# Performance work log

Measured on AMD Instinct MI355X. Metric: run time of the kernel, lower is better.

## Reference

```python
import jax, jax.numpy as jnp
import numpy as np

B, S, D, H = 4, 2048, 512, 8
HD = D // H  # head_size = 64


def setup_inputs() -> dict:
    key = jax.random.key(0)
    ks = jax.random.split(key, 11)
    sd = 1.0 / np.sqrt(D)
    return {
        "q": jax.random.normal(ks[0], (B, S, D), jnp.float32),
        "k": jax.random.normal(ks[1], (B, S, D), jnp.float32),
        "v": jax.random.normal(ks[2], (B, S, D), jnp.float32),
        "Wq": jax.random.normal(ks[3], (D, D), jnp.float32) * sd,
        "bq": jnp.zeros((D,), jnp.float32),
        "Wk": jax.random.normal(ks[4], (D, D), jnp.float32) * sd,
        "bk": jnp.zeros((D,), jnp.float32),
        "Wv": jax.random.normal(ks[5], (D, D), jnp.float32) * sd,
        "bv": jnp.zeros((D,), jnp.float32),
        "Wo": jax.random.normal(ks[6], (D, D), jnp.float32) * sd,
        "bo": jnp.zeros((D,), jnp.float32),
    }


def _split_heads(x):
    # [B,S,D] -> [B,H,S,HD]
    return x.reshape(B, S, H, HD).transpose(0, 2, 1, 3)


def reference(q, k, v, Wq, bq, Wk, bk, Wv, bv, Wo, bo):
    qp = _split_heads(q @ Wq.T + bq)
    kp = _split_heads(k @ Wk.T + bk)
    vp = _split_heads(v @ Wv.T + bv)
    scale = 1.0 / jnp.sqrt(jnp.float32(HD))
    scores = jnp.einsum("bhqd,bhkd->bhqk", qp, kp) * scale  # [B,H,S,S]
    weights = jax.nn.softmax(scores, axis=-1)
    ctx = jnp.einsum("bhqk,bhkd->bhqd", weights, vp)
    ctx = ctx.transpose(0, 2, 1, 3).reshape(B, S, D)
    return ctx @ Wo.T + bo
```

## Files before the change

### kernel.cpp

```cpp
#include <hip/hip_runtime.h>
#include <hip/hip_bf16.h>
#include <stdint.h>

#define BB   4
#define SS   2048
#define DDIM 512
#define HH   8
#define HDIM 64
#define MTOT (BB*SS)
#define QSCALE (0.125f * 1.44269504088896340736f)

typedef __bf16 bf16;
typedef __bf16 bf16x8 __attribute__((ext_vector_type(8)));
typedef float  f32x4  __attribute__((ext_vector_type(4)));

__device__ __forceinline__ void gload_lds16(const void* g, void* l) {
    __builtin_amdgcn_global_load_lds(
        (__attribute__((address_space(1))) unsigned int*)(uintptr_t)g,
        (__attribute__((address_space(3))) unsigned int*)l,
        16, 0, 0);
}

__global__ void cvt_kernel(const float* __restrict__ s0, const float* __restrict__ s1,
                           const float* __restrict__ s2, const float* __restrict__ s3,
                           bf16* __restrict__ d0, bf16* __restrict__ d1,
                           bf16* __restrict__ d2, bf16* __restrict__ d3, int n4) {
    const float* s; bf16* d;
    switch (blockIdx.y) {
        case 0:  s = s0; d = d0; break;
        case 1:  s = s1; d = d1; break;
        case 2:  s = s2; d = d2; break;
        default: s = s3; d = d3; break;
    }
    int stride = gridDim.x * blockDim.x;
    for (int i = blockIdx.x * blockDim.x + threadIdx.x; i < n4; i += stride) {
        float4 f = ((const float4*)s)[i];
        union { bf16 h[4]; uint2 u; } o;
        o.h[0] = (bf16)f.x; o.h[1] = (bf16)f.y; o.h[2] = (bf16)f.z; o.h[3] = (bf16)f.w;
        ((uint2*)d)[i] = o.u;
    }
}

#define GEMM_BODY(A_, W_, K_)                                                    \
    __shared__ bf16 As[128 * 32];                                                \
    __shared__ bf16 Bs[128 * 32];                                                \
    const int tid = threadIdx.x;                                                 \
    const int w = tid >> 6, lane = tid & 63;                                     \
    const int c15 = lane & 15, quad = lane >> 4;                                 \
    const int mblk = blockIdx.x * 128, nblk = blockIdx.y * 128;                  \
    const int wm = (w & 1) * 64, wn = (w >> 1) * 64;                             \
    f32x4 acc[4][4] = {};                                                        \
    const bf16* Ablk = (A_) + (size_t)mblk * (K_);                               \
    const bf16* Bblk = (W_) + (size_t)nblk * (K_);                               \
    const int srow = w * 32 + (lane >> 2);                                       \
    const int scol = (lane & 3) * 8;                                             \
    for (int kt = 0; kt < (K_); kt += 32) {                                      \
        __syncthreads();                                                         \
        gload_lds16(Ablk + (size_t)srow * (K_) + kt + scol, &As[(w*32) * 32]);   \
        gload_lds16(Ablk + (size_t)(srow+16) * (K_) + kt + scol, &As[(w*32+16)*32]); \
        gload_lds16(Bblk + (size_t)srow * (K_) + kt + scol, &Bs[(w*32) * 32]);   \
        gload_lds16(Bblk + (size_t)(srow+16) * (K_) + kt + scol, &Bs[(w*32+16)*32]); \
        __syncthreads();                                                         \
        bf16x8 af[4], bfr[4];                                                    \
        _Pragma("unroll")                                                        \
        for (int i = 0; i < 4; ++i)                                              \
            af[i] = *(const bf16x8*)&As[(wm + i*16 + c15) * 32 + quad * 8];      \
        _Pragma("unroll")                                                        \
        for (int j = 0; j < 4; ++j)                                              \
            bfr[j] = *(const bf16x8*)&Bs[(wn + j*16 + c15) * 32 + quad * 8];     \
        _Pragma("unroll")                                                        \
        for (int i = 0; i < 4; ++i)                                              \
            _Pragma("unroll")                                                    \
            for (int j = 0; j < 4; ++j)                                          \
                acc[i][j] = __builtin_amdgcn_mfma_f32_16x16x32_bf16(             \
                    af[i], bfr[j], acc[i][j], 0, 0, 0);                          \
    }

__global__ __launch_bounds__(256)
void proj_gemm(const bf16* __restrict__ Aq, const bf16* __restrict__ Ak,
               const bf16* __restrict__ Wq, const bf16* __restrict__ Wk,
               const float* __restrict__ bq, const float* __restrict__ bk,
               bf16* __restrict__ Qp, bf16* __restrict__ Kp) {
    const int mode = blockIdx.z;
    const bf16* A  = mode ? Ak : Aq;
    const bf16* Wm = mode ? Wk : Wq;
    const float* bias = mode ? bk : bq;
    GEMM_BODY(A, Wm, DDIM)
    #pragma unroll
    for (int j = 0; j < 4; ++j) {
        const int col = nblk + wn + j * 16 + c15;
        const int h = col >> 6, hd = col & 63;
        const float bval = bias[col];
        #pragma unroll
        for (int i = 0; i < 4; ++i) {
            #pragma unroll
            for (int r = 0; r < 4; ++r) {
                const int row = mblk + wm + i * 16 + quad * 4 + r;
                const int b = row >> 11, s = row & (SS - 1);
                float v = acc[i][j][r] + bval;
                if (mode == 0) {
                    v *= QSCALE;
                    Qp[(((size_t)(b * HH + h)) * SS + s) * HDIM + hd] = (bf16)v;
                } else {
                    Kp[(((size_t)(b * HH + h)) * SS + s) * HDIM + hd] = (bf16)v;
                }
            }
        }
    }
}

__global__ __launch_bounds__(256)
void projv_gemm(const bf16* __restrict__ Wv, const bf16* __restrict__ Av,
                const float* __restrict__ bv, bf16* __restrict__ Vt2) {
    GEMM_BODY(Wv, Av, DDIM)
    #pragma unroll
    for (int i = 0; i < 4; ++i) {
        #pragma unroll
        for (int r = 0; r < 4; ++r) {
            const int row = mblk + wm + i * 16 + quad * 4 + r;
            const float bval = bv[row];
            #pragma unroll
            for (int j = 0; j < 4; ++j) {
                const int col = nblk + wn + j * 16 + c15;
                Vt2[(size_t)row * MTOT + col] = (bf16)(acc[i][j][r] + bval);
            }
        }
    }
}

__global__ __launch_bounds__(256)
void out_gemm(const bf16* __restrict__ A, const bf16* __restrict__ Wo,
              const float* __restrict__ bo, float* __restrict__ Out) {
    GEMM_BODY(A, Wo, DDIM)
    #pragma unroll
    for (int j = 0; j < 4; ++j) {
        const int col = nblk + wn + j * 16 + c15;
        const float bval = bo[col];
        #pragma unroll
        for (int i = 0; i < 4; ++i) {
            #pragma unroll
            for (int r = 0; r < 4; ++r) {
                const int row = mblk + wm + i * 16 + quad * 4 + r;
                Out[(size_t)row * DDIM + col] = acc[i][j][r] + bval;
            }
        }
    }
}

__global__ __launch_bounds__(256, 2)
void attn_kernel(const bf16* __restrict__ Qp, const bf16* __restrict__ Kp,
                 const bf16* __restrict__ Vt2, bf16* __restrict__ Ctx) {
    __shared__ bf16 Klds[128 * 64];
    __shared__ bf16 Vlds[64 * 128];
    __shared__ bf16 Plds[4][32 * 128];

    const int tid = threadIdx.x;
    const int w = tid >> 6, lane = tid & 63;
    const int c15 = lane & 15, quad = lane >> 4;
    const int bh = blockIdx.y;
    const int b = bh >> 3, h = bh & 7;
    const int qbase = blockIdx.x * 128;

    const bf16* Qh = Qp + (size_t)bh * SS * HDIM;
    const bf16* Kh = Kp + (size_t)bh * SS * HDIM;
    const bf16* Vh = Vt2 + (size_t)h * HDIM * MTOT + (size_t)b * SS;

    bf16x8 qf[2][2];
    #pragma unroll
    for (int g = 0; g < 2; ++g) {
        const int qrow = qbase + w * 32 + g * 16 + c15;
        qf[g][0] = *(const bf16x8*)&Qh[(size_t)qrow * HDIM + quad * 8];
        qf[g][1] = *(const bf16x8*)&Qh[(size_t)qrow * HDIM + 32 + quad * 8];
    }

    int koff[4], voff[4];
    #pragma unroll
    for (int ci = 0; ci < 4; ++ci) {
        const int s = (w * 4 + ci) * 64 + lane;
        const int kr = s >> 3, kc = (s & 7) ^ (kr & 7);
        koff[ci] = kr * HDIM + kc * 8;
        const int vr = s >> 4, vc = (s & 15) ^ (vr & 15);
        voff[ci] = vr * MTOT + vc * 8;
    }

    f32x4 oacc[2][4] = {};
    f32x4 lacc[2] = {};
    const bf16 one = (bf16)1.0f;
    const bf16x8 ones = {one, one, one, one, one, one, one, one};
    bf16* Pw = &Plds[w][0];
    const int ksw = c15 & 7;

    for (int kt = 0; kt < SS; kt += 128) {
        __syncthreads();
        const bf16* Ks = Kh + (size_t)kt * HDIM;
        const bf16* Vs = Vh + kt;
        #pragma unroll
        for (int ci = 0; ci < 4; ++ci)
            gload_lds16(Ks + koff[ci], &Klds[(w * 4 + ci) * 512]);
        #pragma unroll
        for (int ci = 0; ci < 4; ++ci)
            gload_lds16(Vs + voff[ci], &Vlds[(w * 4 + ci) * 512]);
        __syncthreads();

        f32x4 sc[2][8];
        #pragma unroll
        for (int nt = 0; nt < 8; ++nt) {
            const int krow = nt * 16 + c15;
            bf16x8 kb0 = *(const bf16x8*)&Klds[(krow * 8 + (quad ^ ksw)) * 8];
            bf16x8 kb1 = *(const bf16x8*)&Klds[(krow * 8 + ((quad + 4) ^ ksw)) * 8];
            #pragma unroll
            for (int g = 0; g < 2; ++g) {
                f32x4 z = {};
                z = __builtin_amdgcn_mfma_f32_16x16x32_bf16(qf[g][0], kb0, z, 0, 0, 0);
                z = __builtin_amdgcn_mfma_f32_16x16x32_bf16(qf[g][1], kb1, z, 0, 0, 0);
                sc[g][nt] = z;
            }
        }

        #pragma unroll
        for (int g = 0; g < 2; ++g)
            #pragma unroll
            for (int nt = 0; nt < 8; ++nt)
                #pragma unroll
                for (int r = 0; r < 4; ++r) {
                    const float p = __builtin_amdgcn_exp2f(sc[g][nt][r]);
                    const int rm = quad * 4 + r;
                    Pw[(g * 16 + rm) * 128 + (((nt * 2 + (c15 >> 3)) ^ rm) * 8) + (c15 & 7)] = (bf16)p;
                }

        bf16x8 pa[2][4];
        #pragma unroll
        for (int g = 0; g < 2; ++g)
            #pragma unroll
            for (int c = 0; c < 4; ++c)
                pa[g][c] = *(const bf16x8*)&Pw[(g * 16 + c15) * 128 + ((c * 4 + quad) ^ c15) * 8];

        #pragma unroll
        for (int g = 0; g < 2; ++g)
            #pragma unroll
            for (int c = 0; c < 4; ++c)
                lacc[g] = __builtin_amdgcn_mfma_f32_16x16x32_bf16(pa[g][c], ones, lacc[g], 0, 0, 0);

        #pragma unroll
        for (int c = 0; c < 4; ++c) {
            #pragma unroll
            for (int j = 0; j < 4; ++j) {
                const int vrow = j * 16 + c15;
                bf16x8 vb = *(const bf16x8*)&Vlds[vrow * 128 + ((c * 4 + quad) ^ c15) * 8];
                oacc[0][j] = __builtin_amdgcn_mfma_f32_16x16x32_bf16(pa[0][c], vb, oacc[0][j], 0, 0, 0);
                oacc[1][j] = __builtin_amdgcn_mfma_f32_16x16x32_bf16(pa[1][c], vb, oacc[1][j], 0, 0, 0);
            }
        }
    }

    bf16* Cb = Ctx + ((size_t)b * SS) * DDIM + (size_t)h * HDIM;
    #pragma unroll
    for (int g = 0; g < 2; ++g)
        #pragma unroll
        for (int r = 0; r < 4; ++r) {
            const int row = qbase + w * 32 + g * 16 + quad * 4 + r;
            const float inv = 1.0f / lacc[g][r];
            #pragma unroll
            for (int j = 0; j < 4; ++j) {
                const int hd = j * 16 + c15;
                Cb[(size_t)row * DDIM + hd] = (bf16)(oacc[g][j][r] * inv);
            }
        }
}

extern "C" void kernel_launch(void* const* d_in, const int* in_sizes, int n_in,
                              void* d_out, int out_size, void* d_ws, size_t ws_size,
                              hipStream_t stream) {
    const float* q  = (const float*)d_in[0];
    const float* k  = (const float*)d_in[1];
    const float* v  = (const float*)d_in[2];
    const float* Wq = (const float*)d_in[3];
    const float* bq = (const float*)d_in[4];
    const float* Wk = (const float*)d_in[5];
    const float* bk = (const float*)d_in[6];
    const float* Wv = (const float*)d_in[7];
    const float* bv = (const float*)d_in[8];
    const float* Wo = (const float*)d_in[9];
    const float* bo = (const float*)d_in[10];
    float* out = (float*)d_out;

    const size_t SZ_T = (size_t)BB * SS * DDIM * 2;
    const size_t SZ_W = (size_t)DDIM * DDIM * 2;
    char* ws = (char*)d_ws;
    bf16* qb  = (bf16*)(ws + 0 * SZ_T);
    bf16* kb  = (bf16*)(ws + 1 * SZ_T);
    bf16* vb  = (bf16*)(ws + 2 * SZ_T);
    bf16* Wqb = (bf16*)(ws + 3 * SZ_T + 0 * SZ_W);
    bf16* Wkb = (bf16*)(ws + 3 * SZ_T + 1 * SZ_W);
    bf16* Wvb = (bf16*)(ws + 3 * SZ_T + 2 * SZ_W);
    bf16* Wob = (bf16*)(ws + 3 * SZ_T + 3 * SZ_W);
    bf16* Qp  = (bf16*)(ws + 3 * SZ_T + 4 * SZ_W);
    bf16* Kp  = (bf16*)(ws + 4 * SZ_T + 4 * SZ_W);
    bf16* Vt2 = (bf16*)(ws + 5 * SZ_T + 4 * SZ_W);
    bf16* ctx = (bf16*)(ws + 6 * SZ_T + 4 * SZ_W);
    const size_t needed = 7 * SZ_T + 4 * SZ_W;
    if (ws_size < needed) return;

    cvt_kernel<<<dim3(512, 3), 256, 0, stream>>>(q, k, v, q, qb, kb, vb, qb,
                                                 (BB * SS * DDIM) / 4);
    cvt_kernel<<<dim3(64, 4), 256, 0, stream>>>(Wq, Wk, Wv, Wo, Wqb, Wkb, Wvb, Wob,
                                                (DDIM * DDIM) / 4);
    proj_gemm<<<dim3(MTOT / 128, DDIM / 128, 2), 256, 0, stream>>>(
        qb, kb, Wqb, Wkb, bq, bk, Qp, Kp);
    projv_gemm<<<dim3(DDIM / 128, MTOT / 128), 256, 0, stream>>>(Wvb, vb, bv, Vt2);
    attn_kernel<<<dim3(SS / 128, BB * HH), 256, 0, stream>>>(Qp, Kp, Vt2, ctx);
    out_gemm<<<dim3(MTOT / 128, DDIM / 128), 256, 0, stream>>>(ctx, Wob, bo, out);
}
```

Baseline: 208.8 us.

## Merge conversion and projection launches, widen GEMM K-tile, keep attention P in registers

Folds the two conversion launches into one and the V projection into the Q/K projection launch as a third grid slice, which cuts launch count and gaps between kernels. The GEMM K-tile is widened from 32 to 64 with an XOR-swizzled LDS layout to halve barrier count and reduce bank conflicts. In attention, the exponentiated scores no longer round-trip through shared memory. An identity-matrix MFMA transposes them into A-operand layout in registers, and V reads are split to match. This adds extra MFMAs and shuffling logic and drops the P LDS buffer, which may raise occupancy.

```diff
diff --git a/kernel.cpp b/kernel.cpp
--- a/kernel.cpp
+++ b/kernel.cpp
@@ -14,6 +14,10 @@
 typedef __bf16 bf16x8 __attribute__((ext_vector_type(8)));
 typedef float  f32x4  __attribute__((ext_vector_type(4)));
 
+__device__ __forceinline__ f32x4 mfma32(bf16x8 a, bf16x8 b, f32x4 c) {
+    return __builtin_amdgcn_mfma_f32_16x16x32_bf16(a, b, c, 0, 0, 0);
+}
+
 __device__ __forceinline__ void gload_lds16(const void* g, void* l) {
     __builtin_amdgcn_global_load_lds(
         (__attribute__((address_space(1))) unsigned int*)(uintptr_t)g,
@@ -21,16 +25,27 @@
         16, 0, 0);
 }
 
-__global__ void cvt_kernel(const float* __restrict__ s0, const float* __restrict__ s1,
-                           const float* __restrict__ s2, const float* __restrict__ s3,
-                           bf16* __restrict__ d0, bf16* __restrict__ d1,
-                           bf16* __restrict__ d2, bf16* __restrict__ d3, int n4) {
-    const float* s; bf16* d;
+__device__ __forceinline__ short bf16bits(float f) {
+    union { __bf16 h; short s; } u; u.h = (__bf16)f; return u.s;
+}
+
+__global__ void cvt_kernel(const float* __restrict__ q, const float* __restrict__ k,
+                           const float* __restrict__ v, const float* __restrict__ w0,
+                           const float* __restrict__ w1, const float* __restrict__ w2,
+                           const float* __restrict__ w3,
+                           bf16* __restrict__ dq, bf16* __restrict__ dk,
+                           bf16* __restrict__ dv, bf16* __restrict__ dw0,
+                           bf16* __restrict__ dw1, bf16* __restrict__ dw2,
+                           bf16* __restrict__ dw3) {
+    const float* s; bf16* d; int n4;
     switch (blockIdx.y) {
-        case 0:  s = s0; d = d0; break;
-        case 1:  s = s1; d = d1; break;
-        case 2:  s = s2; d = d2; break;
-        default: s = s3; d = d3; break;
+        case 0: s = q;  d = dq;  n4 = (BB*SS*DDIM)/4; break;
+        case 1: s = k;  d = dk;  n4 = (BB*SS*DDIM)/4; break;
+        case 2: s = v;  d = dv;  n4 = (BB*SS*DDIM)/4; break;
+        case 3: s = w0; d = dw0; n4 = (DDIM*DDIM)/4; break;
+        case 4: s = w1; d = dw1; n4 = (DDIM*DDIM)/4; break;
+        case 5: s = w2; d = dw2; n4 = (DDIM*DDIM)/4; break;
+        default: s = w3; d = dw3; n4 = (DDIM*DDIM)/4; break;
     }
     int stride = gridDim.x * blockDim.x;
     for (int i = blockIdx.x * blockDim.x + threadIdx.x; i < n4; i += stride) {
@@ -41,88 +56,103 @@
     }
 }
 
-#define GEMM_BODY(A_, W_, K_)                                                    \
-    __shared__ bf16 As[128 * 32];                                                \
-    __shared__ bf16 Bs[128 * 32];                                                \
+#define GEMM_BODY(A_, W_, K_, MB_, NB_)                                          \
+    __shared__ bf16 As[128 * 64];                                                \
+    __shared__ bf16 Bs[128 * 64];                                                \
     const int tid = threadIdx.x;                                                 \
     const int w = tid >> 6, lane = tid & 63;                                     \
     const int c15 = lane & 15, quad = lane >> 4;                                 \
-    const int mblk = blockIdx.x * 128, nblk = blockIdx.y * 128;                  \
+    const int mblk = (MB_), nblk = (NB_);                                        \
     const int wm = (w & 1) * 64, wn = (w >> 1) * 64;                             \
     f32x4 acc[4][4] = {};                                                        \
     const bf16* Ablk = (A_) + (size_t)mblk * (K_);                               \
     const bf16* Bblk = (W_) + (size_t)nblk * (K_);                               \
-    const int srow = w * 32 + (lane >> 2);                                       \
-    const int scol = (lane & 3) * 8;                                             \
-    for (int kt = 0; kt < (K_); kt += 32) {                                      \
+    int g_off[4], l_base[4];                                                     \
+    _Pragma("unroll")                                                            \
+    for (int ci = 0; ci < 4; ++ci) {                                             \
+        const int s = (w * 4 + ci) * 64 + lane;                                  \
+        const int kr = s >> 3, kc = (s & 7) ^ (kr & 7);                          \
+        g_off[ci] = kr * (K_) + kc * 8;                                          \
+        l_base[ci] = (w * 4 + ci) * 512;                                         \
+    }                                                                            \
+    for (int kt = 0; kt < (K_); kt += 64) {                                      \
         __syncthreads();                                                         \
-        gload_lds16(Ablk + (size_t)srow * (K_) + kt + scol, &As[(w*32) * 32]);   \
-        gload_lds16(Ablk + (size_t)(srow+16) * (K_) + kt + scol, &As[(w*32+16)*32]); \
-        gload_lds16(Bblk + (size_t)srow * (K_) + kt + scol, &Bs[(w*32) * 32]);   \
-        gload_lds16(Bblk + (size_t)(srow+16) * (K_) + kt + scol, &Bs[(w*32+16)*32]); \
+        _Pragma("unroll")                                                        \
+        for (int ci = 0; ci < 4; ++ci) {                                         \
+            gload_lds16(Ablk + g_off[ci] + kt, &As[l_base[ci]]);                 \
+            gload_lds16(Bblk + g_off[ci] + kt, &Bs[l_base[ci]]);                 \
+        }                                                                        \
         __syncthreads();                                                         \
-        bf16x8 af[4], bfr[4];                                                    \
         _Pragma("unroll")                                                        \
-        for (int i = 0; i < 4; ++i)                                              \
-            af[i] = *(const bf16x8*)&As[(wm + i*16 + c15) * 32 + quad * 8];      \
-        _Pragma("unroll")                                                        \
-        for (int j = 0; j < 4; ++j)                                              \
-            bfr[j] = *(const bf16x8*)&Bs[(wn + j*16 + c15) * 32 + quad * 8];     \
-        _Pragma("unroll")                                                        \
-        for (int i = 0; i < 4; ++i)                                              \
+        for (int hh = 0; hh < 2; ++hh) {                                         \
+            bf16x8 af[4], bfr[4];                                                \
             _Pragma("unroll")                                                    \
-            for (int j = 0; j < 4; ++j)                                          \
-                acc[i][j] = __builtin_amdgcn_mfma_f32_16x16x32_bf16(             \
-                    af[i], bfr[j], acc[i][j], 0, 0, 0);                          \
+            for (int i = 0; i < 4; ++i) {                                        \
+                const int row = wm + i * 16 + c15;                               \
+                af[i] = *(const bf16x8*)&As[row * 64 + (((hh * 4 + quad) ^ (row & 7)) * 8)]; \
+            }                                                                    \
+            _Pragma("unroll")                                                    \
+            for (int j = 0; j < 4; ++j) {                                        \
+                const int row = wn + j * 16 + c15;                               \
+                bfr[j] = *(const bf16x8*)&Bs[row * 64 + (((hh * 4 + quad) ^ (row & 7)) * 8)]; \
+            }                                                                    \
+            _Pragma("unroll")                                                    \
+            for (int i = 0; i < 4; ++i)                                          \
+                _Pragma("unroll")                                                \
+                for (int j = 0; j < 4; ++j)                                      \
+                    acc[i][j] = mfma32(af[i], bfr[j], acc[i][j]);                \
+        }                                                                        \
     }
 
 __global__ __launch_bounds__(256)
 void proj_gemm(const bf16* __restrict__ Aq, const bf16* __restrict__ Ak,
+               const bf16* __restrict__ Av,
                const bf16* __restrict__ Wq, const bf16* __restrict__ Wk,
+               const bf16* __restrict__ Wv,
                const float* __restrict__ bq, const float* __restrict__ bk,
-               bf16* __restrict__ Qp, bf16* __restrict__ Kp) {
+               const float* __restrict__ bv,
+               bf16* __restrict__ Qp, bf16* __restrict__ Kp, bf16* __restrict__ Vt2) {
     const int mode = blockIdx.z;
-    const bf16* A  = mode ? Ak : Aq;
-    const bf16* Wm = mode ? Wk : Wq;
-    const float* bias = mode ? bk : bq;
-    GEMM_BODY(A, Wm, DDIM)
-    #pragma unroll
-    for (int j = 0; j < 4; ++j) {
-        const int col = nblk + wn + j * 16 + c15;
-        const int h = col >> 6, hd = col & 63;
-        const float bval = bias[col];
+    const bf16* A;  const bf16* Wm; const float* bias;
+    int mb, nb;
+    if (mode == 0)      { A = Aq; Wm = Wq; bias = bq; mb = blockIdx.x * 128; nb = blockIdx.y * 128; }
+    else if (mode == 1) { A = Ak; Wm = Wk; bias = bk; mb = blockIdx.x * 128; nb = blockIdx.y * 128; }
+    else {
+        const int id = blockIdx.y * 64 + blockIdx.x;
+        A = Wv; Wm = Av; bias = bv; mb = (id & 3) * 128; nb = (id >> 2) * 128;
+    }
+    GEMM_BODY(A, Wm, DDIM, mb, nb)
+    if (mode == 2) {
         #pragma unroll
         for (int i = 0; i < 4; ++i) {
             #pragma unroll
             for (int r = 0; r < 4; ++r) {
                 const int row = mblk + wm + i * 16 + quad * 4 + r;
-                const int b = row >> 11, s = row & (SS - 1);
-                float v = acc[i][j][r] + bval;
-                if (mode == 0) {
-                    v *= QSCALE;
-                    Qp[(((size_t)(b * HH + h)) * SS + s) * HDIM + hd] = (bf16)v;
-                } else {
-                    Kp[(((size_t)(b * HH + h)) * SS + s) * HDIM + hd] = (bf16)v;
+                const float bval = bias[row];
+                #pragma unroll
+                for (int j = 0; j < 4; ++j) {
+                    const int col = nblk + wn + j * 16 + c15;
+                    Vt2[(size_t)row * MTOT + col] = (bf16)(acc[i][j][r] + bval);
                 }
             }
         }
-    }
-}
-
-__global__ __launch_bounds__(256)
-void projv_gemm(const bf16* __restrict__ Wv, const bf16* __restrict__ Av,
-                const float* __restrict__ bv, bf16* __restrict__ Vt2) {
-    GEMM_BODY(Wv, Av, DDIM)
-    #pragma unroll
-    for (int i = 0; i < 4; ++i) {
-        #pragma unroll
-        for (int r = 0; r < 4; ++r) {
-            const int row = mblk + wm + i * 16 + quad * 4 + r;
-            const float bval = bv[row];
-            #pragma unroll
-            for (int j = 0; j < 4; ++j) {
-                const int col = nblk + wn + j * 16 + c15;
-                Vt2[(size_t)row * MTOT + col] = (bf16)(acc[i][j][r] + bval);
+    } else {
+        #pragma unroll
+        for (int j = 0; j < 4; ++j) {
+            const int col = nblk + wn + j * 16 + c15;
+            const int h = col >> 6, hd = col & 63;
+            const float bval = bias[col];
+            #pragma unroll
+            for (int i = 0; i < 4; ++i) {
+                #pragma unroll
+                for (int r = 0; r < 4; ++r) {
+                    const int row = mblk + wm + i * 16 + quad * 4 + r;
+                    const int b = row >> 11, s = row & (SS - 1);
+                    float v = acc[i][j][r] + bval;
+                    if (mode == 0) v *= QSCALE;
+                    bf16* dst = (mode == 0) ? Qp : Kp;
+                    dst[(((size_t)(b * HH + h)) * SS + s) * HDIM + hd] = (bf16)v;
+                }
             }
         }
     }
@@ -131,7 +161,7 @@
 __global__ __launch_bounds__(256)
 void out_gemm(const bf16* __restrict__ A, const bf16* __restrict__ Wo,
               const float* __restrict__ bo, float* __restrict__ Out) {
-    GEMM_BODY(A, Wo, DDIM)
+    GEMM_BODY(A, Wo, DDIM, blockIdx.x * 128, blockIdx.y * 128)
     #pragma unroll
     for (int j = 0; j < 4; ++j) {
         const int col = nblk + wn + j * 16 + c15;
@@ -152,7 +182,6 @@
                  const bf16* __restrict__ Vt2, bf16* __restrict__ Ctx) {
     __shared__ bf16 Klds[128 * 64];
     __shared__ bf16 Vlds[64 * 128];
-    __shared__ bf16 Plds[4][32 * 128];
 
     const int tid = threadIdx.x;
     const int w = tid >> 6, lane = tid & 63;
@@ -183,11 +212,16 @@
         voff[ci] = vr * MTOT + vc * 8;
     }
 
+    union FragS { short s[8]; bf16x8 v; };
+    FragS idf, ones8;
+    #pragma unroll
+    for (int j = 0; j < 8; ++j) {
+        idf.s[j] = (j < 4 && quad * 4 + j == c15) ? (short)0x3F80 : (short)0;
+        ones8.s[j] = (short)0x3F80;
+    }
+
     f32x4 oacc[2][4] = {};
     f32x4 lacc[2] = {};
-    const bf16 one = (bf16)1.0f;
-    const bf16x8 ones = {one, one, one, one, one, one, one, one};
-    bf16* Pw = &Plds[w][0];
     const int ksw = c15 & 7;
 
     for (int kt = 0; kt < SS; kt += 128) {
@@ -202,7 +236,7 @@
             gload_lds16(Vs + voff[ci], &Vlds[(w * 4 + ci) * 512]);
         __syncthreads();
 
-        f32x4 sc[2][8];
+        FragS paf[2][4];
         #pragma unroll
         for (int nt = 0; nt < 8; ++nt) {
             const int krow = nt * 16 + c15;
@@ -211,44 +245,36 @@
             #pragma unroll
             for (int g = 0; g < 2; ++g) {
                 f32x4 z = {};
-                z = __builtin_amdgcn_mfma_f32_16x16x32_bf16(qf[g][0], kb0, z, 0, 0, 0);
-                z = __builtin_amdgcn_mfma_f32_16x16x32_bf16(qf[g][1], kb1, z, 0, 0, 0);
-                sc[g][nt] = z;
-            }
-        }
-
-        #pragma unroll
-        for (int g = 0; g < 2; ++g)
-            #pragma unroll
-            for (int nt = 0; nt < 8; ++nt)
+                z = mfma32(qf[g][0], kb0, z);
+                z = mfma32(qf[g][1], kb1, z);
+                FragS pk;
                 #pragma unroll
-                for (int r = 0; r < 4; ++r) {
-                    const float p = __builtin_amdgcn_exp2f(sc[g][nt][r]);
-                    const int rm = quad * 4 + r;
-                    Pw[(g * 16 + rm) * 128 + (((nt * 2 + (c15 >> 3)) ^ rm) * 8) + (c15 & 7)] = (bf16)p;
-                }
-
-        bf16x8 pa[2][4];
-        #pragma unroll
-        for (int g = 0; g < 2; ++g)
-            #pragma unroll
-            for (int c = 0; c < 4; ++c)
-                pa[g][c] = *(const bf16x8*)&Pw[(g * 16 + c15) * 128 + ((c * 4 + quad) ^ c15) * 8];
-
-        #pragma unroll
-        for (int g = 0; g < 2; ++g)
-            #pragma unroll
-            for (int c = 0; c < 4; ++c)
-                lacc[g] = __builtin_amdgcn_mfma_f32_16x16x32_bf16(pa[g][c], ones, lacc[g], 0, 0, 0);
-
-        #pragma unroll
-        for (int c = 0; c < 4; ++c) {
+                for (int r = 0; r < 4; ++r)
+                    pk.s[r] = bf16bits(__builtin_amdgcn_exp2f(z[r]));
+                pk.s[4] = pk.s[5] = pk.s[6] = pk.s[7] = 0;
+                f32x4 zero = {};
+                f32x4 t = mfma32(pk.v, idf.v, zero);
+                const int half = (nt & 1) * 4;
+                #pragma unroll
+                for (int r = 0; r < 4; ++r)
+                    paf[g][nt >> 1].s[half + r] = bf16bits(t[r]);
+            }
+        }
+
+        #pragma unroll
+        for (int t = 0; t < 4; ++t) {
+            lacc[0] = mfma32(paf[0][t].v, ones8.v, lacc[0]);
+            lacc[1] = mfma32(paf[1][t].v, ones8.v, lacc[1]);
             #pragma unroll
             for (int j = 0; j < 4; ++j) {
-                const int vrow = j * 16 + c15;
-                bf16x8 vb = *(const bf16x8*)&Vlds[vrow * 128 + ((c * 4 + quad) ^ c15) * 8];
-                oacc[0][j] = __builtin_amdgcn_mfma_f32_16x16x32_bf16(pa[0][c], vb, oacc[0][j], 0, 0, 0);
-                oacc[1][j] = __builtin_amdgcn_mfma_f32_16x16x32_bf16(pa[1][c], vb, oacc[1][j], 0, 0, 0);
+                const int row = j * 16 + c15;
+                union { uint2 u[2]; bf16x8 v; } vb;
+                vb.u[0] = *(const uint2*)&Vlds[row * 128 +
+                          (((4 * t + (quad >> 1)) ^ c15) * 8) + (quad & 1) * 4];
+                vb.u[1] = *(const uint2*)&Vlds[row * 128 +
+                          (((4 * t + 2 + (quad >> 1)) ^ c15) * 8) + (quad & 1) * 4];
+                oacc[0][j] = mfma32(paf[0][t].v, vb.v, oacc[0][j]);
+                oacc[1][j] = mfma32(paf[1][t].v, vb.v, oacc[1][j]);
             }
         }
     }
@@ -301,13 +327,10 @@
     const size_t needed = 7 * SZ_T + 4 * SZ_W;
     if (ws_size < needed) return;
 
-    cvt_kernel<<<dim3(512, 3), 256, 0, stream>>>(q, k, v, q, qb, kb, vb, qb,
-                                                 (BB * SS * DDIM) / 4);
-    cvt_kernel<<<dim3(64, 4), 256, 0, stream>>>(Wq, Wk, Wv, Wo, Wqb, Wkb, Wvb, Wob,
-                                                (DDIM * DDIM) / 4);
-    proj_gemm<<<dim3(MTOT / 128, DDIM / 128, 2), 256, 0, stream>>>(
-        qb, kb, Wqb, Wkb, bq, bk, Qp, Kp);
-    projv_gemm<<<dim3(DDIM / 128, MTOT / 128), 256, 0, stream>>>(Wvb, vb, bv, Vt2);
+    cvt_kernel<<<dim3(512, 7), 256, 0, stream>>>(q, k, v, Wq, Wk, Wv, Wo,
+                                                 qb, kb, vb, Wqb, Wkb, Wvb, Wob);
+    proj_gemm<<<dim3(MTOT / 128, DDIM / 128, 3), 256, 0, stream>>>(
+        qb, kb, vb, Wqb, Wkb, Wvb, bq, bk, bv, Qp, Kp, Vt2);
     attn_kernel<<<dim3(SS / 128, BB * HH), 256, 0, stream>>>(Qp, Kp, Vt2, ctx);
     out_gemm<<<dim3(MTOT / 128, DDIM / 128), 256, 0, stream>>>(ctx, Wob, bo, out);
 }
```

Result: faster. 193.9 us (-7.1%).
